# Performance work log

Hardware: AMD Instinct MI355X
Metric: run time of the kernel (lower is better)

## Reference

```python
import jax, jax.numpy as jnp
import numpy as np

B, S, D = 2, 2048, 1024
N_HEADS = 16
PAT_HEADS = N_HEADS // 4          # MultiheadAttention num_heads = 4
HEAD_DIM = D // PAT_HEADS         # 256
SPARSITY_RATIO = 0.1
MEMORY_PRESSURE = 0.5
NEG_INF = -1e9


def setup_inputs() -> dict:
    key = jax.random.key(0)
    ks = jax.random.split(key, 16)
    sd = 1.0 / np.sqrt(D)
    sh = 1.0 / np.sqrt(D // 4)
    inp = {
        "q": jax.random.normal(ks[0], (B, S, D), jnp.float32),
        "k": jax.random.normal(ks[1], (B, S, D), jnp.float32),
        "v": jax.random.normal(ks[2], (B, S, D), jnp.float32),
        # sparsity predictor: Linear(D, D//4) -> ReLU -> Linear(D//4, 1) -> Sigmoid
        "w1": jax.random.uniform(ks[3], (D, D // 4), jnp.float32, -sd, sd),
        "b1": jax.random.uniform(ks[4], (D // 4,), jnp.float32, -sd, sd),
        "w2": jax.random.uniform(ks[5], (D // 4, 1), jnp.float32, -sh, sh),
        "b2": jax.random.uniform(ks[6], (1,), jnp.float32, -sh, sh),
        # MultiheadAttention in_proj (split) + out_proj, stored [in, out]
        "wq": jax.random.uniform(ks[7], (D, D), jnp.float32, -sd, sd),
        "bq": jnp.zeros((D,), jnp.float32),
        "wk": jax.random.uniform(ks[8], (D, D), jnp.float32, -sd, sd),
        "bk": jnp.zeros((D,), jnp.float32),
        "wv": jax.random.uniform(ks[9], (D, D), jnp.float32, -sd, sd),
        "bv": jnp.zeros((D,), jnp.float32),
        "wo": jax.random.uniform(ks[10], (D, D), jnp.float32, -sd, sd),
        "bo": jnp.zeros((D,), jnp.float32),
    }
    return inp


def reference(q, k, v, w1, b1, w2, b2, wq, bq, wk, bk, wv, bv, wo, bo):
    # learned importance scores -> boolean mask of active tokens
    h = jax.nn.relu(q @ w1 + b1)                       # [B,S,D//4]
    scores = jax.nn.sigmoid(h @ w2 + b2)[..., 0]       # [B,S]
    threshold = SPARSITY_RATIO * (1.0 + MEMORY_PRESSURE)
    mask = scores > threshold                          # [B,S] bool

    # original module flattens all active tokens across batch into ONE
    # sequence and runs MHA over that subset; we express the identical math
    # with a fixed-shape masked attention over the flattened [B*S] tokens.
    N = B * S
    mf = mask.reshape(N)                               # [N]
    qf = q.reshape(N, D)
    kf = k.reshape(N, D)
    vf = v.reshape(N, D)

    qp = (qf @ wq + bq).reshape(N, PAT_HEADS, HEAD_DIM)
    kp = (kf @ wk + bk).reshape(N, PAT_HEADS, HEAD_DIM)
    vp = (vf @ wv + bv).reshape(N, PAT_HEADS, HEAD_DIM)

    scale = 1.0 / np.sqrt(HEAD_DIM)
    logits = jnp.einsum("nhd,mhd->hnm", qp * scale, kp)   # [H,N,N]
    logits = jnp.where(mf[None, None, :], logits, NEG_INF)  # only active keys
    attn = jax.nn.softmax(logits, axis=-1)
    ctx = jnp.einsum("hnm,mhd->nhd", attn, vp).reshape(N, D)
    out = ctx @ wo + bo                                 # [N,D]

    # scatter back: inactive query positions stay zero
    out = jnp.where(mf[:, None], out, 0.0)
    return out.reshape(B, S, D)
```

## Files before the change

kernel.cpp:

```cpp
#include <hip/hip_runtime.h>
#include <hip/hip_bf16.h>
#include <math.h>

typedef __bf16 bf16x8 __attribute__((ext_vector_type(8)));
typedef __bf16 bf16x4 __attribute__((ext_vector_type(4)));
typedef float  f32x4  __attribute__((ext_vector_type(4)));
typedef short  s16x8  __attribute__((ext_vector_type(8)));

#define N_TOK  4096
#define DMODEL 1024
#define NHEAD  4
#define DHEAD  256

__device__ __forceinline__ f32x4 mfma16x16(bf16x8 a, bf16x8 b, f32x4 c) {
    return __builtin_amdgcn_mfma_f32_16x16x32_bf16(a, b, c, 0, 0, 0);
}

__device__ __forceinline__ void gload_lds16(const void* gsrc, void* ldst) {
    __builtin_amdgcn_global_load_lds(
        (const __attribute__((address_space(1))) void*)gsrc,
        (__attribute__((address_space(3))) void*)ldst, 16, 0, 0);
}

struct CvtArgs { const float* src[3]; __bf16* dst[3]; };
__global__ __launch_bounds__(256)
void cvt_bf16_kernel(CvtArgs a)
{
    const float* in = a.src[blockIdx.y];
    __bf16* out = a.dst[blockIdx.y];
    size_t i8 = ((size_t)blockIdx.x * 256 + threadIdx.x) * 8;
    f32x4 t0 = *(const f32x4*)(in + i8);
    f32x4 t1 = *(const f32x4*)(in + i8 + 4);
    bf16x8 b;
    #pragma unroll
    for (int j = 0; j < 4; ++j) { b[j] = (__bf16)t0[j]; b[j + 4] = (__bf16)t1[j]; }
    *(bf16x8*)(out + i8) = b;
}

__device__ __forceinline__ void transposew_body(const float* __restrict__ in,
                                                __bf16* __restrict__ out, int C)
{
    __shared__ __align__(16) __bf16 tile[64 * 72];
    const int tid = threadIdx.x;
    const int r0 = blockIdx.x * 64;
    const int c0 = blockIdx.y * 64;
    if (c0 >= C) return;
    #pragma unroll
    for (int it = 0; it < 4; ++it) {
        int i = tid + it * 256;
        int row = i >> 4, c4 = i & 15;
        f32x4 v = *(const f32x4*)(in + (size_t)(r0 + row) * C + c0 + c4 * 4);
        #pragma unroll
        for (int j = 0; j < 4; ++j)
            tile[(c4 * 4 + j) * 72 + row] = (__bf16)v[j];
    }
    __syncthreads();
    #pragma unroll
    for (int it = 0; it < 2; ++it) {
        int i = tid + it * 256;
        int col = i >> 3, ch = i & 7;
        s16x8 v = *(const s16x8*)(&tile[col * 72 + ch * 8]);
        *(s16x8*)((short*)out + (size_t)(c0 + col) * 1024 + r0 + ch * 8) = v;
    }
}

__global__ __launch_bounds__(256)
void transposew_kernel(const float* __restrict__ in, __bf16* __restrict__ out, int C)
{
    transposew_body(in, out, C);
}

struct TWArgs { const float* src[4]; __bf16* dst[4]; int C[4]; };
__global__ __launch_bounds__(256)
void transposew_batch_kernel(TWArgs a)
{
    int z = blockIdx.z;
    transposew_body(a.src[z], a.dst[z], a.C[z]);
}

template<typename OutT, bool BIASROW>
__global__ __launch_bounds__(256, 2)
void gemm_bt(const __bf16* __restrict__ A, int lda,
             const __bf16* __restrict__ B, int ldb,
             const float* __restrict__ bias,
             OutT* __restrict__ C, int ldc,
             float scale, int relu, const float* __restrict__ rowmask, int K)
{
    __shared__ __align__(16) short As[2][128 * 64];
    __shared__ __align__(16) short Bs[2][64 * 64];
    const int tid  = threadIdx.x;
    const int lane = tid & 63;
    const int wv   = tid >> 6;
    const int c16  = lane & 15;
    const int quad = lane >> 4;
    const int swz  = c16 & 7;
    const int wr   = wv >> 1;
    const int wc   = wv & 1;
    const int m0 = blockIdx.x * 128;
    const int n0 = blockIdx.y * 64;

    f32x4 acc[4][2];
    #pragma unroll
    for (int i = 0; i < 4; ++i)
        #pragma unroll
        for (int j = 0; j < 2; ++j)
            acc[i][j] = (f32x4){0.f, 0.f, 0.f, 0.f};

    const int sRow = lane >> 3;
    const int sCh  = (lane & 7) ^ (sRow & 7);

    auto issue = [&](short* Abuf, short* Bbuf, int k0) {
        #pragma unroll
        for (int g = 0; g < 4; ++g) {
            int row = 32 * wv + 8 * g + sRow;
            const char* src = (const char*)(A + (size_t)(m0 + row) * lda + k0) + sCh * 16;
            gload_lds16(src, (char*)Abuf + (32 * wv + 8 * g) * 128);
        }
        #pragma unroll
        for (int g = 0; g < 2; ++g) {
            int row = 16 * wv + 8 * g + sRow;
            const char* src = (const char*)(B + (size_t)(n0 + row) * ldb + k0) + sCh * 16;
            gload_lds16(src, (char*)Bbuf + (16 * wv + 8 * g) * 128);
        }
    };
    auto compute = [&](const short* Abuf, const short* Bbuf) {
        __builtin_amdgcn_s_setprio(1);
        #pragma unroll
        for (int ks = 0; ks < 2; ++ks) {
            bf16x8 af[4], bfr[2];
            int slot = ((ks * 4 + quad) ^ swz) * 16;
            #pragma unroll
            for (int t = 0; t < 4; ++t)
                af[t] = *(const bf16x8*)((const char*)Abuf + (wr * 64 + t * 16 + c16) * 128 + slot);
            #pragma unroll
            for (int t = 0; t < 2; ++t)
                bfr[t] = *(const bf16x8*)((const char*)Bbuf + (wc * 32 + t * 16 + c16) * 128 + slot);
            #pragma unroll
            for (int tm = 0; tm < 4; ++tm)
                #pragma unroll
                for (int tn = 0; tn < 2; ++tn)
                    acc[tm][tn] = mfma16x16(af[tm], bfr[tn], acc[tm][tn]);
        }
        __builtin_amdgcn_s_setprio(0);
    };

    const int nt = K >> 6;
    issue(As[0], Bs[0], 0);
    __syncthreads();

    #pragma unroll 1
    for (int t = 0; t < nt; t += 2) {
        if (t + 1 < nt) issue(As[1], Bs[1], (t + 1) << 6);
        compute(As[0], Bs[0]);
        __syncthreads();
        if (t + 1 < nt) {
            if (t + 2 < nt) issue(As[0], Bs[0], (t + 2) << 6);
            compute(As[1], Bs[1]);
            __syncthreads();
        }
    }

    #pragma unroll
    for (int tm = 0; tm < 4; ++tm) {
        #pragma unroll
        for (int rr = 0; rr < 4; ++rr) {
            int row = m0 + wr * 64 + tm * 16 + quad * 4 + rr;
            float mk = rowmask ? rowmask[row] : 1.0f;
            float rbv = BIASROW ? bias[row] : 0.0f;
            #pragma unroll
            for (int tn = 0; tn < 2; ++tn) {
                int col = n0 + wc * 32 + tn * 16 + c16;
                float b = BIASROW ? rbv : bias[col];
                float val = (acc[tm][tn][rr] + b) * scale;
                if (relu) val = fmaxf(val, 0.0f);
                val *= mk;
                C[(size_t)row * ldc + col] = (OutT)val;
            }
        }
    }
}

__global__ void score_mask_kernel(const __bf16* __restrict__ h,
                                  const float* __restrict__ w2,
                                  const float* __restrict__ b2,
                                  float* __restrict__ maskf)
{
    int lane = threadIdx.x & 63;
    int tok  = blockIdx.x * 4 + (threadIdx.x >> 6);
    const __bf16* hr = h + (size_t)tok * 256;
    float s = 0.f;
    #pragma unroll
    for (int j = 0; j < 4; ++j) {
        int c = j * 64 + lane;
        s += (float)hr[c] * w2[c];
    }
    #pragma unroll
    for (int o = 1; o < 64; o <<= 1) s += __shfl_xor(s, o);
    if (lane == 0) {
        float x = s + b2[0];
        maskf[tok] = (x > -1.7346010553881064f) ? 1.0f : 0.0f;
    }
}

__global__ __launch_bounds__(512, 1)
void attn_kernel(const __bf16* __restrict__ qp, const __bf16* __restrict__ kp,
                 const __bf16* __restrict__ vpT, const float* __restrict__ maskf,
                 __bf16* __restrict__ O0, __bf16* __restrict__ O1,
                 float* __restrict__ lbuf)
{
    __shared__ __align__(16) short Ks[2][64 * 256];
    __shared__ __align__(16) short Vs[2][256 * 64];
    __shared__ __align__(16) short PsA[8 * 16 * 64];

    const int tid  = threadIdx.x;
    const int lane = tid & 63;
    const int wv   = tid >> 6;
    const int c16  = lane & 15;
    const int quad = lane >> 4;
    const int swz  = c16 & 7;

    const int d    = blockIdx.x;
    const int orig = ((d & 7) << 5) | (d >> 3);
    const int qb   = orig & 31;
    const int head = (orig >> 5) & 3;
    const int ksp  = orig >> 7;
    const int kbase = ksp * 2048;
    const int kend  = kbase + 2048;
    const int q0   = qb * 128 + wv * 16;
    short* Ps = PsA + wv * 16 * 64;
    __bf16* Ob = ksp ? O1 : O0;

    bf16x8 qf[8];
    #pragma unroll
    for (int c = 0; c < 8; ++c)
        qf[c] = *(const bf16x8*)(qp + (size_t)(q0 + c16) * DMODEL + head * DHEAD + c * 32 + quad * 8);

    f32x4 o[16];
    #pragma unroll
    for (int t = 0; t < 16; ++t) o[t] = (f32x4){0.f, 0.f, 0.f, 0.f};
    float psum[4] = {0.f, 0.f, 0.f, 0.f};

    const int kRow0 = wv * 8 + (lane >> 5);
    const int kCh   = lane & 31;
    const int vRow0 = wv * 32 + (lane >> 3);
    const int vCh   = (lane & 7) ^ ((lane >> 3) & 7);

    auto issue = [&](int buf, int n0) {
        #pragma unroll
        for (int g = 0; g < 4; ++g) {
            int key = kRow0 + g * 2;
            int c   = kCh ^ (key & 7);
            const char* src = (const char*)(kp + (size_t)(n0 + key) * DMODEL + head * DHEAD) + c * 16;
            gload_lds16(src, (char*)Ks[buf] + (wv * 8 + g * 2) * 512);
        }
        #pragma unroll
        for (int g = 0; g < 4; ++g) {
            int row = vRow0 + g * 8;
            const char* src = (const char*)(vpT + (size_t)(head * DHEAD + row) * N_TOK + n0) + vCh * 16;
            gload_lds16(src, (char*)Vs[buf] + (wv * 32 + g * 8) * 128);
        }
    };

    issue(0, kbase);
    __syncthreads();
    int cur = 0;

    #pragma unroll 1
    for (int n0 = kbase; n0 < kend; n0 += 64) {
        if (n0 + 64 < kend) issue(cur ^ 1, n0 + 64);
        const short* Kb = Ks[cur];
        const short* Vb = Vs[cur];

        f32x4 s[4];
        #pragma unroll
        for (int kt = 0; kt < 4; ++kt) s[kt] = (f32x4){0.f, 0.f, 0.f, 0.f};
        __builtin_amdgcn_s_setprio(1);
        #pragma unroll
        for (int c = 0; c < 8; ++c)
            #pragma unroll
            for (int kt = 0; kt < 4; ++kt) {
                bf16x8 bfr = *(const bf16x8*)(&Kb[(kt * 16 + c16) * 256 + (((c * 4 + quad) ^ swz) << 3)]);
                s[kt] = mfma16x16(qf[c], bfr, s[kt]);
            }
        __builtin_amdgcn_s_setprio(0);

        #pragma unroll
        for (int kt = 0; kt < 4; ++kt) {
            float biasv = (maskf[n0 + kt * 16 + c16] - 1.0f) * 1e9f;
            #pragma unroll
            for (int r = 0; r < 4; ++r) {
                float p = __expf(s[kt][r] + biasv);
                psum[r] += p;
                int qrow = quad * 4 + r;
                int ch = (kt * 2 + (c16 >> 3)) ^ (qrow & 7);
                *(__bf16*)&Ps[qrow * 64 + ch * 8 + swz] = (__bf16)p;
            }
        }

        __builtin_amdgcn_s_waitcnt(0xc07f);

        __builtin_amdgcn_s_setprio(1);
        #pragma unroll
        for (int kstep = 0; kstep < 2; ++kstep) {
            bf16x8 pf = *(const bf16x8*)(&Ps[c16 * 64 + (((kstep * 4 + quad) ^ swz) << 3)]);
            #pragma unroll
            for (int t = 0; t < 16; ++t) {
                bf16x8 vf = *(const bf16x8*)(&Vb[(t * 16 + c16) * 64 + (((kstep * 4 + quad) ^ swz) << 3)]);
                o[t] = mfma16x16(pf, vf, o[t]);
            }
        }
        __builtin_amdgcn_s_setprio(0);
        __syncthreads();
        cur ^= 1;
    }

    float inv[4];
    #pragma unroll
    for (int r = 0; r < 4; ++r) {
        float t = psum[r];
        t += __shfl_xor(t, 1);
        t += __shfl_xor(t, 2);
        t += __shfl_xor(t, 4);
        t += __shfl_xor(t, 8);
        if (c16 == 0)
            lbuf[(size_t)(ksp * NHEAD + head) * N_TOK + q0 + quad * 4 + r] = t;
        inv[r] = 1.0f / t;
    }
    #pragma unroll
    for (int t = 0; t < 16; ++t)
        #pragma unroll
        for (int r = 0; r < 4; ++r) {
            float val = o[t][r] * inv[r];
            Ob[(size_t)(q0 + quad * 4 + r) * DMODEL + head * DHEAD + t * 16 + c16] = (__bf16)val;
        }
}

__global__ void combine_kernel(const __bf16* __restrict__ O0,
                               const __bf16* __restrict__ O1,
                               const float* __restrict__ lbuf,
                               __bf16* __restrict__ out)
{
    int idx  = blockIdx.x * 256 + threadIdx.x;
    int tok  = idx >> 7;
    int g    = idx & 127;
    int head = g >> 5;
    float a = lbuf[(size_t)head * N_TOK + tok];
    float b = lbuf[(size_t)(NHEAD + head) * N_TOK + tok];
    float w0 = a / (a + b);
    float w1 = 1.0f - w0;
    size_t off = (size_t)tok * DMODEL + g * 8;
    bf16x8 x = *(const bf16x8*)(O0 + off);
    bf16x8 y = *(const bf16x8*)(O1 + off);
    bf16x8 z;
    #pragma unroll
    for (int j = 0; j < 8; ++j) z[j] = (__bf16)(w0 * (float)x[j] + w1 * (float)y[j]);
    *(bf16x8*)(out + off) = z;
}

extern "C" void kernel_launch(void* const* d_in, const int* in_sizes, int n_in,
                              void* d_out, int out_size, void* d_ws, size_t ws_size,
                              hipStream_t stream)
{
    (void)in_sizes; (void)n_in; (void)out_size;
    const float* q  = (const float*)d_in[0];
    const float* k  = (const float*)d_in[1];
    const float* v  = (const float*)d_in[2];
    const float* w1 = (const float*)d_in[3];
    const float* b1 = (const float*)d_in[4];
    const float* w2 = (const float*)d_in[5];
    const float* b2 = (const float*)d_in[6];
    const float* wq = (const float*)d_in[7];
    const float* bq = (const float*)d_in[8];
    const float* wk = (const float*)d_in[9];
    const float* bk = (const float*)d_in[10];
    const float* wvw = (const float*)d_in[11];
    const float* bv = (const float*)d_in[12];
    const float* wo = (const float*)d_in[13];
    const float* bo = (const float*)d_in[14];

    if (ws_size < 35667968u + 8388608u + 131072u) return;

    char* ws = (char*)d_ws;
    float*  maskf = (float*)ws;
    __bf16* hbuf  = (__bf16*)(ws + 16384);
    __bf16* qp    = (__bf16*)(ws + 16384 + 2097152);
    __bf16* kpb   = qp  + 4194304;
    __bf16* vpT   = kpb + 4194304;
    __bf16* ctx   = vpT + 4194304;
    __bf16* O1    = (__bf16*)(ws + 35667968u);
    float*  lbuf  = (float*)(ws + 35667968u + 8388608u);

    __bf16* wqT = (__bf16*)d_out;
    __bf16* wkT = wqT + 1048576;
    __bf16* wvT = wkT + 1048576;
    __bf16* w1T = wvT + 1048576;
    __bf16* vbf = (__bf16*)((char*)d_out + 6815744u);
    __bf16* woT = hbuf;
    __bf16* qbf = O1;
    __bf16* kbf = ctx;

    CvtArgs ca;
    ca.src[0] = q;  ca.dst[0] = qbf;
    ca.src[1] = k;  ca.dst[1] = kbf;
    ca.src[2] = v;  ca.dst[2] = vbf;
    cvt_bf16_kernel<<<dim3(2048, 3), 256, 0, stream>>>(ca);

    TWArgs ta;
    ta.src[0] = w1;  ta.dst[0] = w1T;  ta.C[0] = 256;
    ta.src[1] = wq;  ta.dst[1] = wqT;  ta.C[1] = 1024;
    ta.src[2] = wk;  ta.dst[2] = wkT;  ta.C[2] = 1024;
    ta.src[3] = wvw; ta.dst[3] = wvT;  ta.C[3] = 1024;
    transposew_batch_kernel<<<dim3(16, 16, 4), 256, 0, stream>>>(ta);

    gemm_bt<__bf16, false><<<dim3(32, 4), 256, 0, stream>>>(
        qbf, 1024, w1T, 1024, b1, hbuf, 256, 1.0f, 1, nullptr, 1024);
    score_mask_kernel<<<1024, 256, 0, stream>>>(hbuf, w2, b2, maskf);

    transposew_kernel<<<dim3(16, 16), 256, 0, stream>>>(wo, woT, 1024);

    gemm_bt<__bf16, false><<<dim3(32, 16), 256, 0, stream>>>(
        qbf, 1024, wqT, 1024, bq, qp, 1024, 0.0625f, 0, nullptr, 1024);
    gemm_bt<__bf16, false><<<dim3(32, 16), 256, 0, stream>>>(
        kbf, 1024, wkT, 1024, bk, kpb, 1024, 1.0f, 0, nullptr, 1024);
    gemm_bt<__bf16, true><<<dim3(8, 64), 256, 0, stream>>>(
        wvT, 1024, vbf, 1024, bv, vpT, 4096, 1.0f, 0, nullptr, 1024);

    attn_kernel<<<dim3(256), 512, 0, stream>>>(qp, kpb, vpT, maskf, ctx, O1, lbuf);
    combine_kernel<<<2048, 256, 0, stream>>>(ctx, O1, lbuf, ctx);

    gemm_bt<float, false><<<dim3(32, 16), 256, 0, stream>>>(
        ctx, 1024, woT, 1024, bo, (float*)d_out, 1024, 1.0f, 0, maskf, 1024);
}
```

Before: 324.5 us.

## Rewrite attention with 32x32 MFMA, register-resident P, and four-way key split

The attention kernel moves from 16x16x32 to 32x32x16 bf16 MFMA. It computes S^T so that the probabilities stay in registers, exchanged between half-waves with packed bf16 conversions and a lane shuffle, which removes the LDS round trip for P. The key range is split four ways instead of two, each wave handles 32 queries, and the occupancy hint rises to 2 blocks per CU. The mask is applied multiplicatively after exp, and per-split outputs are left unnormalized so combine divides by the summed row totals. Workspace buffers are reused (O2/O3 in the output, lbuf over hbuf), which requires moving the wo transpose after combine; this adds register pressure and more partial-output traffic.

```diff
diff --git a/kernel.cpp b/kernel.cpp
--- a/kernel.cpp
+++ b/kernel.cpp
@@ -5,6 +5,7 @@
 typedef __bf16 bf16x8 __attribute__((ext_vector_type(8)));
 typedef __bf16 bf16x4 __attribute__((ext_vector_type(4)));
 typedef float  f32x4  __attribute__((ext_vector_type(4)));
+typedef float  f32x16 __attribute__((ext_vector_type(16)));
 typedef short  s16x8  __attribute__((ext_vector_type(8)));
 
 #define N_TOK  4096
@@ -14,6 +15,14 @@
 
 __device__ __forceinline__ f32x4 mfma16x16(bf16x8 a, bf16x8 b, f32x4 c) {
     return __builtin_amdgcn_mfma_f32_16x16x32_bf16(a, b, c, 0, 0, 0);
+}
+__device__ __forceinline__ f32x16 mfma32(bf16x8 a, bf16x8 b, f32x16 c) {
+    return __builtin_amdgcn_mfma_f32_32x32x16_bf16(a, b, c, 0, 0, 0);
+}
+__device__ __forceinline__ unsigned cvtpk(float lo, float hi) {
+    unsigned r;
+    asm("v_cvt_pk_bf16_f32 %0, %1, %2" : "=v"(r) : "v"(lo), "v"(hi));
+    return r;
 }
 
 __device__ __forceinline__ void gload_lds16(const void* gsrc, void* ldst) {
@@ -202,43 +211,44 @@
     }
 }
 
-__global__ __launch_bounds__(512, 1)
+__global__ __launch_bounds__(512, 2)
 void attn_kernel(const __bf16* __restrict__ qp, const __bf16* __restrict__ kp,
                  const __bf16* __restrict__ vpT, const float* __restrict__ maskf,
                  __bf16* __restrict__ O0, __bf16* __restrict__ O1,
+                 __bf16* __restrict__ O2, __bf16* __restrict__ O3,
                  float* __restrict__ lbuf)
 {
     __shared__ __align__(16) short Ks[2][64 * 256];
     __shared__ __align__(16) short Vs[2][256 * 64];
-    __shared__ __align__(16) short PsA[8 * 16 * 64];
 
     const int tid  = threadIdx.x;
     const int lane = tid & 63;
     const int wv   = tid >> 6;
-    const int c16  = lane & 15;
-    const int quad = lane >> 4;
-    const int swz  = c16 & 7;
+    const int l31  = lane & 31;
+    const int hi   = lane >> 5;
+    const int swz  = lane & 7;
 
     const int d    = blockIdx.x;
-    const int orig = ((d & 7) << 5) | (d >> 3);
-    const int qb   = orig & 31;
-    const int head = (orig >> 5) & 3;
-    const int ksp  = orig >> 7;
-    const int kbase = ksp * 2048;
-    const int kend  = kbase + 2048;
-    const int q0   = qb * 128 + wv * 16;
-    short* Ps = PsA + wv * 16 * 64;
-    __bf16* Ob = ksp ? O1 : O0;
-
-    bf16x8 qf[8];
-    #pragma unroll
-    for (int c = 0; c < 8; ++c)
-        qf[c] = *(const bf16x8*)(qp + (size_t)(q0 + c16) * DMODEL + head * DHEAD + c * 32 + quad * 8);
-
-    f32x4 o[16];
-    #pragma unroll
-    for (int t = 0; t < 16; ++t) o[t] = (f32x4){0.f, 0.f, 0.f, 0.f};
-    float psum[4] = {0.f, 0.f, 0.f, 0.f};
+    const int g    = d & 7;
+    const int t    = d >> 3;
+    const int head = g >> 1;
+    const int ksp  = (g & 1) * 2 + (t >> 4);
+    const int qb   = t & 15;
+    const int kbase = ksp * 1024;
+    const int q0w  = qb * 256 + wv * 32;
+    __bf16* Ob = (ksp == 0) ? O0 : (ksp == 1) ? O1 : (ksp == 2) ? O2 : O3;
+
+    bf16x8 qf[16];
+    #pragma unroll
+    for (int c = 0; c < 16; ++c)
+        qf[c] = *(const bf16x8*)(qp + (size_t)(q0w + l31) * DMODEL + head * DHEAD + c * 16 + hi * 8);
+
+    f32x16 o[8];
+    #pragma unroll
+    for (int i = 0; i < 8; ++i)
+        #pragma unroll
+        for (int r = 0; r < 16; ++r) o[i][r] = 0.f;
+    f32x4 psum4 = (f32x4){0.f, 0.f, 0.f, 0.f};
 
     const int kRow0 = wv * 8 + (lane >> 5);
     const int kCh   = lane & 31;
@@ -247,17 +257,17 @@
 
     auto issue = [&](int buf, int n0) {
         #pragma unroll
-        for (int g = 0; g < 4; ++g) {
-            int key = kRow0 + g * 2;
+        for (int gg = 0; gg < 4; ++gg) {
+            int key = kRow0 + gg * 2;
             int c   = kCh ^ (key & 7);
             const char* src = (const char*)(kp + (size_t)(n0 + key) * DMODEL + head * DHEAD) + c * 16;
-            gload_lds16(src, (char*)Ks[buf] + (wv * 8 + g * 2) * 512);
-        }
-        #pragma unroll
-        for (int g = 0; g < 4; ++g) {
-            int row = vRow0 + g * 8;
+            gload_lds16(src, (char*)Ks[buf] + (wv * 8 + gg * 2) * 512);
+        }
+        #pragma unroll
+        for (int gg = 0; gg < 4; ++gg) {
+            int row = vRow0 + gg * 8;
             const char* src = (const char*)(vpT + (size_t)(head * DHEAD + row) * N_TOK + n0) + vCh * 16;
-            gload_lds16(src, (char*)Vs[buf] + (wv * 32 + g * 8) * 128);
+            gload_lds16(src, (char*)Vs[buf] + (wv * 32 + gg * 8) * 128);
         }
     };
 
@@ -266,77 +276,85 @@
     int cur = 0;
 
     #pragma unroll 1
-    for (int n0 = kbase; n0 < kend; n0 += 64) {
-        if (n0 + 64 < kend) issue(cur ^ 1, n0 + 64);
+    for (int n0 = kbase; n0 < kbase + 1024; n0 += 64) {
+        if (n0 + 64 < kbase + 1024) issue(cur ^ 1, n0 + 64);
         const short* Kb = Ks[cur];
         const short* Vb = Vs[cur];
 
-        f32x4 s[4];
-        #pragma unroll
-        for (int kt = 0; kt < 4; ++kt) s[kt] = (f32x4){0.f, 0.f, 0.f, 0.f};
-        __builtin_amdgcn_s_setprio(1);
-        #pragma unroll
-        for (int c = 0; c < 8; ++c)
-            #pragma unroll
-            for (int kt = 0; kt < 4; ++kt) {
-                bf16x8 bfr = *(const bf16x8*)(&Kb[(kt * 16 + c16) * 256 + (((c * 4 + quad) ^ swz) << 3)]);
-                s[kt] = mfma16x16(qf[c], bfr, s[kt]);
+        #pragma unroll
+        for (int kb = 0; kb < 2; ++kb) {
+            f32x16 s;
+            #pragma unroll
+            for (int r = 0; r < 16; ++r) s[r] = 0.f;
+            __builtin_amdgcn_s_setprio(1);
+            #pragma unroll
+            for (int c = 0; c < 16; ++c) {
+                bf16x8 kf = *(const bf16x8*)((const char*)Kb + (kb * 32 + l31) * 512 + (((c * 2 + hi) ^ swz) << 4));
+                s = mfma32(kf, qf[c], s);
             }
-        __builtin_amdgcn_s_setprio(0);
-
-        #pragma unroll
-        for (int kt = 0; kt < 4; ++kt) {
-            float biasv = (maskf[n0 + kt * 16 + c16] - 1.0f) * 1e9f;
-            #pragma unroll
-            for (int r = 0; r < 4; ++r) {
-                float p = __expf(s[kt][r] + biasv);
-                psum[r] += p;
-                int qrow = quad * 4 + r;
-                int ch = (kt * 2 + (c16 >> 3)) ^ (qrow & 7);
-                *(__bf16*)&Ps[qrow * 64 + ch * 8 + swz] = (__bf16)p;
+            __builtin_amdgcn_s_setprio(0);
+
+            float p[16];
+            #pragma unroll
+            for (int gq = 0; gq < 4; ++gq) {
+                f32x4 mv = *(const f32x4*)(maskf + n0 + kb * 32 + gq * 8 + hi * 4);
+                #pragma unroll
+                for (int j = 0; j < 4; ++j) {
+                    float pv = __expf(s[gq * 4 + j]) * mv[j];
+                    p[gq * 4 + j] = pv;
+                    psum4[j] += pv;
+                }
             }
-        }
-
-        __builtin_amdgcn_s_waitcnt(0xc07f);
-
-        __builtin_amdgcn_s_setprio(1);
-        #pragma unroll
-        for (int kstep = 0; kstep < 2; ++kstep) {
-            bf16x8 pf = *(const bf16x8*)(&Ps[c16 * 64 + (((kstep * 4 + quad) ^ swz) << 3)]);
-            #pragma unroll
-            for (int t = 0; t < 16; ++t) {
-                bf16x8 vf = *(const bf16x8*)(&Vb[(t * 16 + c16) * 64 + (((kstep * 4 + quad) ^ swz) << 3)]);
-                o[t] = mfma16x16(pf, vf, o[t]);
+
+            unsigned A = cvtpk(p[0], p[1]),  B = cvtpk(p[2], p[3]);
+            unsigned C = cvtpk(p[4], p[5]),  D = cvtpk(p[6], p[7]);
+            unsigned E = cvtpk(p[8], p[9]),  F = cvtpk(p[10], p[11]);
+            unsigned G = cvtpk(p[12], p[13]), H = cvtpk(p[14], p[15]);
+            unsigned y0 = (unsigned)__shfl_xor((int)(hi ? A : C), 32);
+            unsigned y1 = (unsigned)__shfl_xor((int)(hi ? B : D), 32);
+            unsigned y2 = (unsigned)__shfl_xor((int)(hi ? E : G), 32);
+            unsigned y3 = (unsigned)__shfl_xor((int)(hi ? F : H), 32);
+            union { unsigned u[4]; bf16x8 v; } plo, phi;
+            plo.u[0] = hi ? y0 : A;  plo.u[1] = hi ? y1 : B;
+            plo.u[2] = hi ? C  : y0; plo.u[3] = hi ? D  : y1;
+            phi.u[0] = hi ? y2 : E;  phi.u[1] = hi ? y3 : F;
+            phi.u[2] = hi ? G  : y2; phi.u[3] = hi ? H  : y3;
+
+            __builtin_amdgcn_s_setprio(1);
+            #pragma unroll
+            for (int ks2 = 0; ks2 < 2; ++ks2) {
+                bf16x8 pa = ks2 ? phi.v : plo.v;
+                int chunk = (kb * 2 + ks2) * 2 + hi;
+                #pragma unroll
+                for (int dhb = 0; dhb < 8; ++dhb) {
+                    bf16x8 vf = *(const bf16x8*)((const char*)Vb + (dhb * 32 + l31) * 128 + ((chunk ^ swz) << 4));
+                    o[dhb] = mfma32(pa, vf, o[dhb]);
+                }
             }
-        }
-        __builtin_amdgcn_s_setprio(0);
+            __builtin_amdgcn_s_setprio(0);
+        }
         __syncthreads();
         cur ^= 1;
     }
 
-    float inv[4];
-    #pragma unroll
-    for (int r = 0; r < 4; ++r) {
-        float t = psum[r];
-        t += __shfl_xor(t, 1);
-        t += __shfl_xor(t, 2);
-        t += __shfl_xor(t, 4);
-        t += __shfl_xor(t, 8);
-        if (c16 == 0)
-            lbuf[(size_t)(ksp * NHEAD + head) * N_TOK + q0 + quad * 4 + r] = t;
-        inv[r] = 1.0f / t;
-    }
-    #pragma unroll
-    for (int t = 0; t < 16; ++t)
-        #pragma unroll
-        for (int r = 0; r < 4; ++r) {
-            float val = o[t][r] * inv[r];
-            Ob[(size_t)(q0 + quad * 4 + r) * DMODEL + head * DHEAD + t * 16 + c16] = (__bf16)val;
+    float psum = (psum4[0] + psum4[1]) + (psum4[2] + psum4[3]);
+    float tot = psum + __shfl_xor(psum, 32);
+    if (lane < 32)
+        lbuf[(size_t)(ksp * NHEAD + head) * N_TOK + q0w + l31] = tot;
+
+    #pragma unroll
+    for (int dhb = 0; dhb < 8; ++dhb)
+        #pragma unroll
+        for (int r = 0; r < 16; ++r) {
+            int qrow = (r & 3) + 8 * (r >> 2) + 4 * hi;
+            Ob[(size_t)(q0w + qrow) * DMODEL + head * DHEAD + dhb * 32 + l31] = (__bf16)o[dhb][r];
         }
 }
 
 __global__ void combine_kernel(const __bf16* __restrict__ O0,
                                const __bf16* __restrict__ O1,
+                               const __bf16* __restrict__ O2,
+                               const __bf16* __restrict__ O3,
                                const float* __restrict__ lbuf,
                                __bf16* __restrict__ out)
 {
@@ -344,16 +362,20 @@
     int tok  = idx >> 7;
     int g    = idx & 127;
     int head = g >> 5;
-    float a = lbuf[(size_t)head * N_TOK + tok];
-    float b = lbuf[(size_t)(NHEAD + head) * N_TOK + tok];
-    float w0 = a / (a + b);
-    float w1 = 1.0f - w0;
+    float l0 = lbuf[(size_t)(0 * NHEAD + head) * N_TOK + tok];
+    float l1 = lbuf[(size_t)(1 * NHEAD + head) * N_TOK + tok];
+    float l2 = lbuf[(size_t)(2 * NHEAD + head) * N_TOK + tok];
+    float l3 = lbuf[(size_t)(3 * NHEAD + head) * N_TOK + tok];
+    float inv = 1.0f / (l0 + l1 + l2 + l3);
     size_t off = (size_t)tok * DMODEL + g * 8;
-    bf16x8 x = *(const bf16x8*)(O0 + off);
-    bf16x8 y = *(const bf16x8*)(O1 + off);
+    bf16x8 a = *(const bf16x8*)(O0 + off);
+    bf16x8 b = *(const bf16x8*)(O1 + off);
+    bf16x8 c = *(const bf16x8*)(O2 + off);
+    bf16x8 dd = *(const bf16x8*)(O3 + off);
     bf16x8 z;
     #pragma unroll
-    for (int j = 0; j < 8; ++j) z[j] = (__bf16)(w0 * (float)x[j] + w1 * (float)y[j]);
+    for (int j = 0; j < 8; ++j)
+        z[j] = (__bf16)((((float)a[j] + (float)b[j]) + ((float)c[j] + (float)dd[j])) * inv);
     *(bf16x8*)(out + off) = z;
 }
 
@@ -383,18 +405,20 @@
     char* ws = (char*)d_ws;
     float*  maskf = (float*)ws;
     __bf16* hbuf  = (__bf16*)(ws + 16384);
+    float*  lbuf  = (float*)(ws + 16384);
     __bf16* qp    = (__bf16*)(ws + 16384 + 2097152);
     __bf16* kpb   = qp  + 4194304;
     __bf16* vpT   = kpb + 4194304;
     __bf16* ctx   = vpT + 4194304;
     __bf16* O1    = (__bf16*)(ws + 35667968u);
-    float*  lbuf  = (float*)(ws + 35667968u + 8388608u);
 
     __bf16* wqT = (__bf16*)d_out;
     __bf16* wkT = wqT + 1048576;
     __bf16* wvT = wkT + 1048576;
     __bf16* w1T = wvT + 1048576;
     __bf16* vbf = (__bf16*)((char*)d_out + 6815744u);
+    __bf16* O2  = (__bf16*)d_out;
+    __bf16* O3  = (__bf16*)((char*)d_out + 8388608u);
     __bf16* woT = hbuf;
     __bf16* qbf = O1;
     __bf16* kbf = ctx;
@@ -416,8 +440,6 @@
         qbf, 1024, w1T, 1024, b1, hbuf, 256, 1.0f, 1, nullptr, 1024);
     score_mask_kernel<<<1024, 256, 0, stream>>>(hbuf, w2, b2, maskf);
 
-    transposew_kernel<<<dim3(16, 16), 256, 0, stream>>>(wo, woT, 1024);
-
     gemm_bt<__bf16, false><<<dim3(32, 16), 256, 0, stream>>>(
         qbf, 1024, wqT, 1024, bq, qp, 1024, 0.0625f, 0, nullptr, 1024);
     gemm_bt<__bf16, false><<<dim3(32, 16), 256, 0, stream>>>(
@@ -425,9 +447,10 @@
     gemm_bt<__bf16, true><<<dim3(8, 64), 256, 0, stream>>>(
         wvT, 1024, vbf, 1024, bv, vpT, 4096, 1.0f, 0, nullptr, 1024);
 
-    attn_kernel<<<dim3(256), 512, 0, stream>>>(qp, kpb, vpT, maskf, ctx, O1, lbuf);
-    combine_kernel<<<2048, 256, 0, stream>>>(ctx, O1, lbuf, ctx);
-
+    attn_kernel<<<dim3(256), 512, 0, stream>>>(qp, kpb, vpT, maskf, ctx, O1, O2, O3, lbuf);
+    combine_kernel<<<2048, 256, 0, stream>>>(ctx, O1, O2, O3, lbuf, ctx);
+
+    transposew_kernel<<<dim3(16, 16), 256, 0, stream>>>(wo, woT, 1024);
     gemm_bt<float, false><<<dim3(32, 16), 256, 0, stream>>>(
         ctx, 1024, woT, 1024, bo, (float*)d_out, 1024, 1.0f, 0, maskf, 1024);
 }
```

Result: slower. 388.7 us (+19.8%).
